# Performance work log

Hardware: AMD Instinct MI355X
Metric: run time of the kernel (lower is better)

## Reference

```python
import jax, jax.numpy as jnp
import numpy as np

S, B, H, K = 4096, 1, 2048, 2  # seq_len, batch (forced to 1 by the view()), hidden_dim, conv kernel
EMBED = K * K                  # embed_dim must equal kernel_size**2
THRESHOLD = 0.0


def setup_inputs() -> dict:
    key = jax.random.key(0)
    k0, k1, k2 = jax.random.split(key, 3)
    inputs = jax.random.normal(k0, (S, B, EMBED), dtype=jnp.float32)
    # ConvFilter params: Conv2d(1,1,K) on a KxK patch == dot with flattened kernel + bias
    conv_w = jax.random.normal(k1, (EMBED,), dtype=jnp.float32) * 0.5
    conv_b = jnp.zeros((1,), dtype=jnp.float32)
    # Four gate Linears (1+H -> H) stacked column-wise into one (1+H, 4H) matmul
    # order: forget | input | update | output  (same math as 4 separate nn.Linear)
    w_gates = (jax.random.normal(k2, (1 + H, 4 * H), dtype=jnp.float32)
               / np.sqrt(1.0 + H)).astype(jnp.float32)
    b_gates = jnp.zeros((4 * H,), dtype=jnp.float32)
    return {"inputs": inputs, "conv_w": conv_w, "conv_b": conv_b,
            "w_gates": w_gates, "b_gates": b_gates}


def reference(inputs, conv_w, conv_b, w_gates, b_gates):
    S_, B_, _ = inputs.shape
    H_ = w_gates.shape[1] // 4

    # Conv preprocess (vectorized over all timesteps): each (K,K) token patch
    # -> scalar sigmoid(conv(x) - threshold), then mean over the per-step batch
    # (batch==1, so the mean is the value itself, matching torch's .mean()).
    conv_scalar = jax.nn.sigmoid(inputs @ conv_w + conv_b[0] - THRESHOLD)  # (S, B)
    conv_scalar = jnp.mean(conv_scalar, axis=1, keepdims=True)             # (S, 1)
    conv_out = jnp.broadcast_to(conv_scalar[:, :, None], (S_, B_, 1))      # (S, B, 1)

    hx0 = jnp.zeros((B_, H_), dtype=inputs.dtype)
    cx0 = jnp.zeros((B_, H_), dtype=inputs.dtype)

    def step(carry, c_t):
        hx, cx = carry
        combined = jnp.concatenate([c_t, hx], axis=1)        # (B, 1+H)
        gates = combined @ w_gates + b_gates                  # (B, 4H) fused 4-gate GEMM
        f, i, g, o = jnp.split(gates, 4, axis=1)
        f = jax.nn.sigmoid(f)
        i = jax.nn.sigmoid(i)
        g = jnp.tanh(g)
        o = jax.nn.sigmoid(o)
        cx = f * cx + i * g
        hx = o * jnp.tanh(cx)
        return (hx, cx), hx

    (hx, cx), stacked = jax.lax.scan(step, (hx0, cx0), conv_out)
    return stacked, hx, cx
```

## Files before the change

### kernel.cpp

```cpp
#include <hip/hip_runtime.h>
#include <math.h>

#define S_LEN 4096
#define HID   2048
#define NBLK  256
#define NTHR  512

typedef unsigned int       u32;
typedef unsigned long long u64;


__device__ __forceinline__ float fast_sigmoid(float x) {
    float e = __builtin_amdgcn_exp2f(-1.44269504f * x);
    return __builtin_amdgcn_rcpf(1.0f + e);
}

__global__ __launch_bounds__(NTHR, 2)
void qlstm_persistent(const float* __restrict__ inp,
                      const float* __restrict__ conv_w,
                      const float* __restrict__ conv_b,
                      const float* __restrict__ Wg,
                      const float* __restrict__ bg,
                      float* __restrict__ out,
                      float* __restrict__ ws)
{
    const int b   = blockIdx.x;
    const int tid = threadIdx.x;
    const int l   = tid & 63;
    const int wv  = tid >> 6;

    u32* tb0 = (u32*)ws;
    u32* tb1 = tb0 + HID + 16;

    __shared__ __align__(16) float hx_lds[HID];
    __shared__ __align__(16) float conv_lds[S_LEN];
    __shared__ float gates_lds[32];
    __shared__ float colw0[32];
    __shared__ float colb[32];

    {
        const float cw0 = conv_w[0], cw1 = conv_w[1], cw2 = conv_w[2], cw3 = conv_w[3];
        const float cb  = conv_b[0];
        for (int g = tid; g < S_LEN; g += NTHR) {
            float4 x = ((const float4*)inp)[g];
            float v = x.x*cw0 + x.y*cw1 + x.z*cw2 + x.w*cw3 + cb;
            conv_lds[g] = fast_sigmoid(v);
        }
    }
    ((float4*)hx_lds)[tid] = make_float4(0.f, 0.f, 0.f, 0.f);

    int jcol[4];
    #pragma unroll
    for (int c = 0; c < 4; ++c) {
        int cgi  = 4*wv + c;
        int gate = cgi >> 3;
        int mi   = cgi & 7;
        jcol[c]  = (gate << 11) + (b * 8 + mi);
    }
    if (l == 0) {
        #pragma unroll
        for (int c = 0; c < 4; ++c) {
            int cgi = 4*wv + c;
            colw0[cgi] = Wg[jcol[c]];
            colb[cgi]  = bg[jcol[c]];
        }
    }

    float wreg[4][32];
    #pragma unroll
    for (int j = 0; j < 8; ++j)
        #pragma unroll
        for (int r = 0; r < 4; ++r) {
            const float* rowp = Wg + (size_t)(1 + 4*l + 256*j + r) * 8192;
            #pragma unroll
            for (int c = 0; c < 4; ++c)
                wreg[c][4*j + r] = rowp[jcol[c]];
        }
    asm volatile("" ::: "memory");

    float cx = 0.0f;
    const int m_out = b * 8 + tid;
    const int e0 = tid * 4;

    u32 v0 = 0, v1 = 0, v2 = 0, v3 = 0;
    unsigned pend = 0;

    for (int t = 0; t < S_LEN; ++t) {
        u32* tb = (t & 1) ? tb1 : tb0;
        u32* tn = (t & 1) ? tb0 : tb1;

        if (pend) {
            const u32 want = ((u32)(t + 1) & 3u) ^ 2u;
            int slept = 0;
            do {
                if (slept) __builtin_amdgcn_s_sleep(1);
                slept = 1;
                u64 qa = 0, qb = 0;
                if (pend & 3u)
                    qa = __hip_atomic_load((const u64*)(tb + e0),
                                           __ATOMIC_RELAXED, __HIP_MEMORY_SCOPE_AGENT);
                if (pend & 12u)
                    qb = __hip_atomic_load((const u64*)(tb + e0 + 2),
                                           __ATOMIC_RELAXED, __HIP_MEMORY_SCOPE_AGENT);
                u32 c0 = (u32)qa, c1 = (u32)(qa >> 32);
                u32 c2 = (u32)qb, c3 = (u32)(qb >> 32);
                if ((pend & 1u) && (c0 & 3u) == want) { v0 = c0; pend &= ~1u; }
                if ((pend & 2u) && (c1 & 3u) == want) { v1 = c1; pend &= ~2u; }
                if ((pend & 4u) && (c2 & 3u) == want) { v2 = c2; pend &= ~4u; }
                if ((pend & 8u) && (c3 & 3u) == want) { v3 = c3; pend &= ~8u; }
            } while (pend);
            uint4 st;
            st.x = v0 & ~3u; st.y = v1 & ~3u; st.z = v2 & ~3u; st.w = v3 & ~3u;
            ((uint4*)hx_lds)[tid] = st;
        }
        __syncthreads();

        const float4* hl = (const float4*)hx_lds;
        float acc0 = 0.f, acc1 = 0.f, acc2 = 0.f, acc3 = 0.f;
        #pragma unroll
        for (int j = 0; j < 8; ++j) {
            float4 h = hl[l + 64*j];
            acc0 = fmaf(h.x, wreg[0][4*j+0], acc0);
            acc1 = fmaf(h.x, wreg[1][4*j+0], acc1);
            acc2 = fmaf(h.x, wreg[2][4*j+0], acc2);
            acc3 = fmaf(h.x, wreg[3][4*j+0], acc3);
            acc0 = fmaf(h.y, wreg[0][4*j+1], acc0);
            acc1 = fmaf(h.y, wreg[1][4*j+1], acc1);
            acc2 = fmaf(h.y, wreg[2][4*j+1], acc2);
            acc3 = fmaf(h.y, wreg[3][4*j+1], acc3);
            acc0 = fmaf(h.z, wreg[0][4*j+2], acc0);
            acc1 = fmaf(h.z, wreg[1][4*j+2], acc1);
            acc2 = fmaf(h.z, wreg[2][4*j+2], acc2);
            acc3 = fmaf(h.z, wreg[3][4*j+2], acc3);
            acc0 = fmaf(h.w, wreg[0][4*j+3], acc0);
            acc1 = fmaf(h.w, wreg[1][4*j+3], acc1);
            acc2 = fmaf(h.w, wreg[2][4*j+3], acc2);
            acc3 = fmaf(h.w, wreg[3][4*j+3], acc3);
        }
        #pragma unroll
        for (int off = 32; off; off >>= 1) {
            acc0 += __shfl_down(acc0, off, 64);
            acc1 += __shfl_down(acc1, off, 64);
            acc2 += __shfl_down(acc2, off, 64);
            acc3 += __shfl_down(acc3, off, 64);
        }
        if (l == 0) {
            gates_lds[4*wv + 0] = acc0;
            gates_lds[4*wv + 1] = acc1;
            gates_lds[4*wv + 2] = acc2;
            gates_lds[4*wv + 3] = acc3;
        }
        __syncthreads();

        if (wv == 0) __builtin_amdgcn_s_setprio(1);
        if (tid < 8) {
            float ct = conv_lds[t];
            float fg = gates_lds[tid]      + ct*colw0[tid]      + colb[tid];
            float ig = gates_lds[8 + tid]  + ct*colw0[8 + tid]  + colb[8 + tid];
            float gg = gates_lds[16 + tid] + ct*colw0[16 + tid] + colb[16 + tid];
            float og = gates_lds[24 + tid] + ct*colw0[24 + tid] + colb[24 + tid];
            float f  = fast_sigmoid(fg);
            float ii = fast_sigmoid(ig);
            float gv = 2.0f * fast_sigmoid(2.0f * gg) - 1.0f;
            float o  = fast_sigmoid(og);
            cx = f * cx + ii * gv;
            float hx = o * (2.0f * fast_sigmoid(2.0f * cx) - 1.0f);
            u32 word = (__float_as_uint(hx) & ~3u) | (((u32)(t + 2) & 3u) ^ 2u);
            __hip_atomic_store(&tn[m_out], word,
                               __ATOMIC_RELAXED, __HIP_MEMORY_SCOPE_AGENT);
            out[(size_t)t * HID + m_out] = hx;
            if (t == S_LEN - 1) {
                out[(size_t)S_LEN * HID + m_out]       = hx;
                out[(size_t)S_LEN * HID + HID + m_out] = cx;
            }
        }
        if (wv == 0) __builtin_amdgcn_s_setprio(0);

        pend = 0xFu;
    }
}

extern "C" void kernel_launch(void* const* d_in, const int* in_sizes, int n_in,
                              void* d_out, int out_size, void* d_ws, size_t ws_size,
                              hipStream_t stream) {
    const float* inp    = (const float*)d_in[0];
    const float* conv_w = (const float*)d_in[1];
    const float* conv_b = (const float*)d_in[2];
    const float* Wg     = (const float*)d_in[3];
    const float* bg     = (const float*)d_in[4];
    float* out = (float*)d_out;
    float* ws  = (float*)d_ws;

    void* args[] = {(void*)&inp, (void*)&conv_w, (void*)&conv_b,
                    (void*)&Wg, (void*)&bg, (void*)&out, (void*)&ws};
    hipLaunchCooperativeKernel((void*)qlstm_persistent,
                               dim3(NBLK), dim3(NTHR), args, 0, stream);
}
```

Measured before the change: 13.46 ms.

## Interleave double-buffered hx exchange per block and poll with single dwordx4 loads

Changes the global hx exchange layout so that each block's two parity slots sit side by side in one 64-byte line (16 words per block, 8 per parity), instead of two separate HID-sized buffers. Polling becomes a single inline-asm global_load_dwordx4 with sc0 sc1 cache bypass that retries until all four values carry the expected tag. The sleep backoff and the per-element pending mask are removed. This aims to cut the latency of the per-step cross-block synchronization, at the cost of more aggressive spinning and reliance on hand-written cache-control asm.

Result: faster. 11.45 ms (-14.9%).

```diff
diff --git a/kernel.cpp b/kernel.cpp
--- a/kernel.cpp
+++ b/kernel.cpp
@@ -8,6 +8,7 @@
 
 typedef unsigned int       u32;
 typedef unsigned long long u64;
+typedef unsigned u32x4 __attribute__((ext_vector_type(4)));
 
 
 __device__ __forceinline__ float fast_sigmoid(float x) {
@@ -29,8 +30,7 @@
     const int l   = tid & 63;
     const int wv  = tid >> 6;
 
-    u32* tb0 = (u32*)ws;
-    u32* tb1 = tb0 + HID + 16;
+    u32* tbl = (u32*)ws;
 
     __shared__ __align__(16) float hx_lds[HID];
     __shared__ __align__(16) float conv_lds[S_LEN];
@@ -76,42 +76,30 @@
             for (int c = 0; c < 4; ++c)
                 wreg[c][4*j + r] = rowp[jcol[c]];
         }
-    asm volatile("" ::: "memory");
 
     float cx = 0.0f;
     const int m_out = b * 8 + tid;
-    const int e0 = tid * 4;
 
-    u32 v0 = 0, v1 = 0, v2 = 0, v3 = 0;
-    unsigned pend = 0;
+    const u32* poll_base = tbl + (tid >> 1) * 16 + (tid & 1) * 4;
+    u32* pub_base = tbl + b * 16 + tid;
 
     for (int t = 0; t < S_LEN; ++t) {
-        u32* tb = (t & 1) ? tb1 : tb0;
-        u32* tn = (t & 1) ? tb0 : tb1;
-
-        if (pend) {
+        if (t) {
             const u32 want = ((u32)(t + 1) & 3u) ^ 2u;
-            int slept = 0;
+            const u32* pp = poll_base + ((t & 1) << 3);
+            u32x4 q;
+            u32 miss;
             do {
-                if (slept) __builtin_amdgcn_s_sleep(1);
-                slept = 1;
-                u64 qa = 0, qb = 0;
-                if (pend & 3u)
-                    qa = __hip_atomic_load((const u64*)(tb + e0),
-                                           __ATOMIC_RELAXED, __HIP_MEMORY_SCOPE_AGENT);
-                if (pend & 12u)
-                    qb = __hip_atomic_load((const u64*)(tb + e0 + 2),
-                                           __ATOMIC_RELAXED, __HIP_MEMORY_SCOPE_AGENT);
-                u32 c0 = (u32)qa, c1 = (u32)(qa >> 32);
-                u32 c2 = (u32)qb, c3 = (u32)(qb >> 32);
-                if ((pend & 1u) && (c0 & 3u) == want) { v0 = c0; pend &= ~1u; }
-                if ((pend & 2u) && (c1 & 3u) == want) { v1 = c1; pend &= ~2u; }
-                if ((pend & 4u) && (c2 & 3u) == want) { v2 = c2; pend &= ~4u; }
-                if ((pend & 8u) && (c3 & 3u) == want) { v3 = c3; pend &= ~8u; }
-            } while (pend);
-            uint4 st;
-            st.x = v0 & ~3u; st.y = v1 & ~3u; st.z = v2 & ~3u; st.w = v3 & ~3u;
-            ((uint4*)hx_lds)[tid] = st;
+                asm volatile("global_load_dwordx4 %0, %1, off sc0 sc1\n\t"
+                             "s_waitcnt vmcnt(0)"
+                             : "=v"(q) : "v"(pp) : "memory");
+                miss = ((q[0] ^ want) & 3u) | ((q[1] ^ want) & 3u)
+                     | ((q[2] ^ want) & 3u) | ((q[3] ^ want) & 3u);
+            } while (miss);
+            u32x4 st;
+            st[0] = q[0] & ~3u; st[1] = q[1] & ~3u;
+            st[2] = q[2] & ~3u; st[3] = q[3] & ~3u;
+            ((u32x4*)hx_lds)[tid] = st;
         }
         __syncthreads();
 
@@ -166,7 +154,7 @@
             cx = f * cx + ii * gv;
             float hx = o * (2.0f * fast_sigmoid(2.0f * cx) - 1.0f);
             u32 word = (__float_as_uint(hx) & ~3u) | (((u32)(t + 2) & 3u) ^ 2u);
-            __hip_atomic_store(&tn[m_out], word,
+            __hip_atomic_store(pub_base + (((t + 1) & 1) << 3), word,
                                __ATOMIC_RELAXED, __HIP_MEMORY_SCOPE_AGENT);
             out[(size_t)t * HID + m_out] = hx;
             if (t == S_LEN - 1) {
@@ -175,8 +163,6 @@
             }
         }
         if (wv == 0) __builtin_amdgcn_s_setprio(0);
-
-        pend = 0xFu;
     }
 }
 
```
